# Optimization experiments

Hardware: AMD Instinct MI355X
Metric: run time of the kernel (lower is better)

Reference implementation:

```python
import jax, jax.numpy as jnp
import numpy as np

H = 1152      # embed_dim
NH = 16       # num heads
HD = H // NH  # head_dim = 72
SCALE = HD ** -0.5
B, S = 16, 729


def fake_quant(x, bits):
    """Symmetric per-tensor fake quantize-dequantize with straight-through estimator."""
    qmax = 2.0 ** (bits - 1) - 1.0
    scale = jnp.maximum(jnp.max(jnp.abs(x)), 1e-8) / qmax
    q = jnp.clip(jnp.round(x / scale), -qmax - 1.0, qmax) * scale
    return x + jax.lax.stop_gradient(q - x)  # STE


def fq_linear(x, W, b):
    # FakeQuantLinear: 8-bit fake-quant on activations and weights, fp accumulate
    return fake_quant(x, 8) @ fake_quant(W, 8).T + b


def setup_inputs() -> dict:
    key = jax.random.key(0)
    ks = jax.random.split(key, 9)
    std = H ** -0.5
    return {
        "hidden_states": jax.random.normal(ks[0], (B, S, H), jnp.float32),
        "Wq": jax.random.normal(ks[1], (H, H), jnp.float32) * std,
        "bq": jax.random.normal(ks[2], (H,), jnp.float32) * 0.02,
        "Wk": jax.random.normal(ks[3], (H, H), jnp.float32) * std,
        "bk": jax.random.normal(ks[4], (H,), jnp.float32) * 0.02,
        "Wv": jax.random.normal(ks[5], (H, H), jnp.float32) * std,
        "bv": jax.random.normal(ks[6], (H,), jnp.float32) * 0.02,
        "Wo": jax.random.normal(ks[7], (H, H), jnp.float32) * std,
        "bo": jax.random.normal(ks[8], (H,), jnp.float32) * 0.02,
    }


def reference(hidden_states, Wq, bq, Wk, bk, Wv, bv, Wo, bo):
    b, s, _ = hidden_states.shape
    q = fq_linear(hidden_states, Wq, bq).reshape(b, s, NH, HD).transpose(0, 2, 1, 3)
    k = fq_linear(hidden_states, Wk, bk).reshape(b, s, NH, HD).transpose(0, 2, 1, 3)
    v = fq_linear(hidden_states, Wv, bv).reshape(b, s, NH, HD).transpose(0, 2, 1, 3)
    # FakeQuantMatmul(8, 16): 8-bit quant on both matmul inputs, 16-bit quant on output
    attn = fake_quant(
        jnp.einsum("bhqd,bhkd->bhqk", fake_quant(q, 8), fake_quant(k, 8)), 16
    ) * SCALE
    # FakeQuantSoftmax(quant_bits=16): softmax then 16-bit fake quant
    attn = fake_quant(jax.nn.softmax(attn, axis=-1), 16)
    # FakeQuantMatmul(None, 8): no input quant, 8-bit output quant
    out = fake_quant(jnp.einsum("bhqk,bhkd->bhqd", attn, v), 8)
    out = out.transpose(0, 2, 1, 3).reshape(b, s, H)
    return fq_linear(out, Wo, bo)
```

## Files before the change

kernel.cpp:

```cpp
#include <hip/hip_runtime.h>
#include <math.h>

#define Hdim 1152
#define NHd  16
#define HDd  72
#define Bd   16
#define Sd   729
#define Ntok (Bd*Sd)
#define BHd  (Bd*NHd)
#define SCALE_F 0.117851130197757934f
#define LOG2E 1.44269504088896340736f

#define KFTB 8192
#define VFT 10240

#define SL_X 0
#define SL_WQ 1
#define SL_WK 2
#define SL_WV 3
#define SL_WO 4
#define SL_Q 5
#define SL_K 6
#define SL_LOGIT 8
#define SL_LMIN 9
#define SL_O 10

typedef short short8 __attribute__((ext_vector_type(8)));
typedef short short4v __attribute__((ext_vector_type(4)));
typedef float f32x4 __attribute__((ext_vector_type(4)));
typedef int int4v __attribute__((ext_vector_type(4)));

static __device__ __forceinline__ unsigned short f2bf(float f) {
  unsigned b = __float_as_uint(f);
  return (unsigned short)((b + 0x7FFFu + ((b >> 16) & 1u)) >> 16);
}
static __device__ __forceinline__ float bf2f(unsigned short u) {
  return __uint_as_float(((unsigned)u) << 16);
}
static __device__ __forceinline__ void atomicMaxF(float* p, float v) {
  atomicMax((unsigned int*)p, __float_as_uint(v));
}
static __device__ __forceinline__ void atomicMinF(float* p, float v) {
  atomicMin((unsigned int*)p, __float_as_uint(v));
}
static __device__ __forceinline__ float qscale(float mx, float qmax) {
  return fmaxf(mx, 1e-8f) / qmax;
}
static __device__ __forceinline__ float fexp2(float x) {
  float r; asm("v_exp_f32 %0, %1" : "=v"(r) : "v"(x)); return r;
}
static __device__ __forceinline__ float flog2(float x) {
  float r; asm("v_log_f32 %0, %1" : "=v"(r) : "v"(x)); return r;
}
static __device__ __forceinline__ short4v pack4(unsigned a, unsigned b, unsigned c, unsigned d) {
  union { unsigned u[2]; short4v s; } t;
  t.u[0] = a | (b << 16);
  t.u[1] = c | (d << 16);
  return t.s;
}
static __device__ __forceinline__ int q8i(float v, float s) {
  return (int)fminf(fmaxf(rintf(v / s), -128.f), 127.f);
}

#if __has_builtin(__builtin_amdgcn_mfma_f32_16x16x16bf16_1k)
#define MFMA16(a, b, c) __builtin_amdgcn_mfma_f32_16x16x16bf16_1k(a, b, c, 0, 0, 0)
#else
static __device__ __forceinline__ f32x4 MFMA16(short4v a, short4v b, f32x4 c) {
  asm("v_mfma_f32_16x16x16_bf16 %0, %1, %2, %0" : "+v"(c) : "v"(a), "v"(b));
  return c;
}
#endif
#if __has_builtin(__builtin_amdgcn_mfma_i32_16x16x64_i8)
#define MFMAI8(a, b, c) __builtin_amdgcn_mfma_i32_16x16x64_i8(a, b, c, 0, 0, 0)
#else
static __device__ __forceinline__ int4v MFMAI8(int4v a, int4v b, int4v c) {
  asm("v_mfma_i32_16x16x64_i8 %0, %1, %2, %0" : "+v"(c) : "v"(a), "v"(b));
  return c;
}
#endif

static __device__ __forceinline__ void gll16(const void* g, void* l) {
  __builtin_amdgcn_global_load_lds((const __attribute__((address_space(1))) void*)g,
                                   (__attribute__((address_space(3))) void*)l, 16, 0, 0);
}

__global__ void k_init(float* slots) {
  int i = threadIdx.x;
  if (i < 32) slots[i] = (i == SL_LMIN) ? __builtin_inff() : 0.0f;
}

__launch_bounds__(256)
__global__ void k_absmax(const float* __restrict__ X, const float* __restrict__ W0,
                         const float* __restrict__ W1, const float* __restrict__ W2,
                         const float* __restrict__ W3, float* slots) {
  int seg = blockIdx.y;
  const float* p; long n; int slot;
  if (seg == 0) { p = X; n = (long)Ntok * Hdim; slot = SL_X; }
  else {
    const float* ws4[4] = {W0, W1, W2, W3};
    p = ws4[seg - 1]; n = (long)Hdim * Hdim; slot = SL_WQ + seg - 1;
  }
  long n4 = n >> 2;
  const float4* p4 = (const float4*)p;
  float m = 0.f;
  for (long i = (long)blockIdx.x * blockDim.x + threadIdx.x; i < n4;
       i += (long)gridDim.x * blockDim.x) {
    float4 v = p4[i];
    m = fmaxf(m, fmaxf(fmaxf(fabsf(v.x), fabsf(v.y)), fmaxf(fabsf(v.z), fabsf(v.w))));
  }
  for (int off = 32; off; off >>= 1) m = fmaxf(m, __shfl_xor(m, off, 64));
  __shared__ float red[4];
  if ((threadIdx.x & 63) == 0) red[threadIdx.x >> 6] = m;
  __syncthreads();
  if (threadIdx.x == 0)
    atomicMaxF(&slots[slot], fmaxf(fmaxf(red[0], red[1]), fmaxf(red[2], red[3])));
}

__launch_bounds__(256)
__global__ void k_quant8i(const float* __restrict__ in, unsigned int* __restrict__ out,
                          long n, const float* __restrict__ slots, int slot) {
  float s = qscale(slots[slot], 127.0f);
  long n4 = n >> 2;
  const float4* in4 = (const float4*)in;
  for (long i = (long)blockIdx.x * blockDim.x + threadIdx.x; i < n4;
       i += (long)gridDim.x * blockDim.x) {
    float4 v = in4[i];
    unsigned a = (unsigned)q8i(v.x, s) & 255u;
    unsigned b = (unsigned)q8i(v.y, s) & 255u;
    unsigned c = (unsigned)q8i(v.z, s) & 255u;
    unsigned d = (unsigned)q8i(v.w, s) & 255u;
    out[i] = a | (b << 8) | (c << 16) | (d << 24);
  }
}

__launch_bounds__(256)
__global__ void k_quant8wi(const float* __restrict__ W0, const float* __restrict__ W1,
                           const float* __restrict__ W2, const float* __restrict__ W3,
                           unsigned int* O0, unsigned int* O1,
                           unsigned int* O2, unsigned int* O3,
                           const float* __restrict__ slots) {
  int seg = blockIdx.y;
  const float* ws4[4] = {W0, W1, W2, W3};
  unsigned int* os4[4] = {O0, O1, O2, O3};
  const float* in = ws4[seg];
  unsigned int* out = os4[seg];
  float s = qscale(slots[SL_WQ + seg], 127.0f);
  long n4 = ((long)Hdim * Hdim) >> 2;
  const float4* in4 = (const float4*)in;
  for (long i = (long)blockIdx.x * blockDim.x + threadIdx.x; i < n4;
       i += (long)gridDim.x * blockDim.x) {
    float4 v = in4[i];
    unsigned a = (unsigned)q8i(v.x, s) & 255u;
    unsigned b = (unsigned)q8i(v.y, s) & 255u;
    unsigned c = (unsigned)q8i(v.z, s) & 255u;
    unsigned d = (unsigned)q8i(v.w, s) & 255u;
    out[i] = a | (b << 8) | (c << 16) | (d << 24);
  }
}

#define GBM 128
#define GBN 128
#define GBK 64
__launch_bounds__(256, 3)
__global__ void k_gemm(const char* __restrict__ A,
                       const char* __restrict__ Bm,
                       const float* __restrict__ bias,
                       float* __restrict__ C,
                       float* slots, int slotA, int slotB, int slotOut) {
  __shared__ char As[GBM][GBK];
  __shared__ char Bs[GBN][GBK];
  __shared__ float red[4];
  int tid = threadIdx.x, lane = tid & 63, wid = tid >> 6;
  int wm = wid >> 1, wn = wid & 1;
  int l15 = lane & 15, l4 = lane >> 4;
  int bM = blockIdx.x, bN = blockIdx.y;
  int4v acc[4][4];
  for (int rf = 0; rf < 4; ++rf)
    for (int cf = 0; cf < 4; ++cf) acc[rf][cf] = int4v{0, 0, 0, 0};

  int srow = lane >> 2, scol = (lane & 3) * 16;
  const char* pa = A + ((long)(bM * GBM + wid * 32) + srow) * Hdim + scol;
  const char* pb = Bm + ((long)(bN * GBN + wid * 32) + srow) * Hdim + scol;

  for (int kt = 0; kt < Hdim / GBK; ++kt) {
    int kb = kt * GBK;
    __syncthreads();
    gll16(pa + kb, &As[wid * 32][0]);
    gll16(pa + kb + 16 * Hdim, &As[wid * 32 + 16][0]);
    gll16(pb + kb, &Bs[wid * 32][0]);
    gll16(pb + kb + 16 * Hdim, &Bs[wid * 32 + 16][0]);
    __syncthreads();
    int4v af[4], bf4[4];
#pragma unroll
    for (int rf = 0; rf < 4; ++rf) af[rf] = *(const int4v*)&As[wm * 64 + rf * 16 + l15][l4 * 16];
#pragma unroll
    for (int cf = 0; cf < 4; ++cf) bf4[cf] = *(const int4v*)&Bs[wn * 64 + cf * 16 + l15][l4 * 16];
#pragma unroll
    for (int rf = 0; rf < 4; ++rf)
#pragma unroll
      for (int cf = 0; cf < 4; ++cf)
        acc[rf][cf] = MFMAI8(af[rf], bf4[cf], acc[rf][cf]);
  }
  float alpha = qscale(slots[slotA], 127.f) * qscale(slots[slotB], 127.f);
  float lmax = 0.f;
#pragma unroll
  for (int cf = 0; cf < 4; ++cf) {
    int col = bN * GBN + wn * 64 + cf * 16 + l15;
    float bv = bias[col];
#pragma unroll
    for (int rf = 0; rf < 4; ++rf)
#pragma unroll
      for (int j = 0; j < 4; ++j) {
        int row = bM * GBM + wm * 64 + rf * 16 + l4 * 4 + j;
        if (row < Ntok) {
          float v = (float)acc[rf][cf][j] * alpha + bv;
          C[(long)row * Hdim + col] = v;
          lmax = fmaxf(lmax, fabsf(v));
        }
      }
  }
  if (slotOut >= 0) {
    for (int off = 32; off; off >>= 1) lmax = fmaxf(lmax, __shfl_xor(lmax, off, 64));
    if ((tid & 63) == 0) red[wid] = lmax;
    __syncthreads();
    if (tid == 0)
      atomicMaxF(&slots[slotOut], fmaxf(fmaxf(red[0], red[1]), fmaxf(red[2], red[3])));
  }
}

__launch_bounds__(256, 3)
__global__ void k_gemm3(const char* __restrict__ A,
                        const char* __restrict__ W0,
                        const char* __restrict__ W1,
                        const char* __restrict__ W2,
                        const float* __restrict__ b0, const float* __restrict__ b1,
                        const float* __restrict__ b2,
                        float* __restrict__ C0, float* __restrict__ C1,
                        float* __restrict__ C2, float* slots) {
  __shared__ char As[GBM][GBK];
  __shared__ char Bs[GBN][GBK];
  __shared__ float red[4];
  int bNg = blockIdx.y;
  int mi = bNg / 9, bN = bNg - mi * 9;
  const char* Bm = mi == 0 ? W0 : (mi == 1 ? W1 : W2);
  const float* bias = mi == 0 ? b0 : (mi == 1 ? b1 : b2);
  float* C = mi == 0 ? C0 : (mi == 1 ? C1 : C2);
  int slotB = SL_WQ + mi;
  int slotOut = mi == 0 ? SL_Q : (mi == 1 ? SL_K : -1);

  int tid = threadIdx.x, lane = tid & 63, wid = tid >> 6;
  int wm = wid >> 1, wn = wid & 1;
  int l15 = lane & 15, l4 = lane >> 4;
  int bM = blockIdx.x;
  int4v acc[4][4];
  for (int rf = 0; rf < 4; ++rf)
    for (int cf = 0; cf < 4; ++cf) acc[rf][cf] = int4v{0, 0, 0, 0};

  int srow = lane >> 2, scol = (lane & 3) * 16;
  const char* pa = A + ((long)(bM * GBM + wid * 32) + srow) * Hdim + scol;
  const char* pb = Bm + ((long)(bN * GBN + wid * 32) + srow) * Hdim + scol;

  for (int kt = 0; kt < Hdim / GBK; ++kt) {
    int kb = kt * GBK;
    __syncthreads();
    gll16(pa + kb, &As[wid * 32][0]);
    gll16(pa + kb + 16 * Hdim, &As[wid * 32 + 16][0]);
    gll16(pb + kb, &Bs[wid * 32][0]);
    gll16(pb + kb + 16 * Hdim, &Bs[wid * 32 + 16][0]);
    __syncthreads();
    int4v af[4], bf4[4];
#pragma unroll
    for (int rf = 0; rf < 4; ++rf) af[rf] = *(const int4v*)&As[wm * 64 + rf * 16 + l15][l4 * 16];
#pragma unroll
    for (int cf = 0; cf < 4; ++cf) bf4[cf] = *(const int4v*)&Bs[wn * 64 + cf * 16 + l15][l4 * 16];
#pragma unroll
    for (int rf = 0; rf < 4; ++rf)
#pragma unroll
      for (int cf = 0; cf < 4; ++cf)
        acc[rf][cf] = MFMAI8(af[rf], bf4[cf], acc[rf][cf]);
  }
  float alpha = qscale(slots[SL_X], 127.f) * qscale(slots[slotB], 127.f);
  float lmax = 0.f;
#pragma unroll
  for (int cf = 0; cf < 4; ++cf) {
    int col = bN * GBN + wn * 64 + cf * 16 + l15;
    float bv = bias[col];
#pragma unroll
    for (int rf = 0; rf < 4; ++rf)
#pragma unroll
      for (int j = 0; j < 4; ++j) {
        int row = bM * GBM + wm * 64 + rf * 16 + l4 * 4 + j;
        if (row < Ntok) {
          float v = (float)acc[rf][cf][j] * alpha + bv;
          C[(long)row * Hdim + col] = v;
          lmax = fmaxf(lmax, fabsf(v));
        }
      }
  }
  if (slotOut >= 0) {
    for (int off = 32; off; off >>= 1) lmax = fmaxf(lmax, __shfl_xor(lmax, off, 64));
    if ((tid & 63) == 0) red[wid] = lmax;
    __syncthreads();
    if (tid == 0)
      atomicMaxF(&slots[slotOut], fmaxf(fmaxf(red[0], red[1]), fmaxf(red[2], red[3])));
  }
}

__launch_bounds__(256)
__global__ void k_kfrag(const float* __restrict__ Kf, char* __restrict__ KF,
                        const float* __restrict__ slots) {
  int kt = blockIdx.x, bh = blockIdx.y;
  int b = bh >> 4, h = bh & 15;
  float s = qscale(slots[SL_K], 127.0f);
  int tid = threadIdx.x, lane = tid & 63, w = tid >> 6;
  int l15 = lane & 15, l4 = lane >> 4;
  long obase = ((long)(bh * 12 + kt)) * KFTB;
#pragma unroll
  for (int i = 0; i < 2; ++i) {
    int p = w * 2 + i;
    int cf = p >> 1, c = p & 1;
    int token = kt * 64 + cf * 16 + l15;
    char ov[16];
#pragma unroll
    for (int j = 0; j < 16; ++j) ov[j] = 0;
    if (token < Sd) {
      const float* src = &Kf[((long)(b * Sd + token)) * Hdim + h * HDd];
      if (c == 0) {
#pragma unroll
        for (int j = 0; j < 16; ++j) ov[j] = (char)q8i(src[l4 * 16 + j], s);
      } else if (l4 == 0) {
#pragma unroll
        for (int j = 0; j < 8; ++j) ov[j] = (char)q8i(src[64 + j], s);
      }
    }
    *(int4v*)&KF[obase + p * 1024 + lane * 16] = *(int4v*)ov;
  }
}

__launch_bounds__(256)
__global__ void k_vsplit(const float* __restrict__ Vf, unsigned short* __restrict__ VF) {
  int kt = blockIdx.x, bh = blockIdx.y;
  int b = bh >> 4, h = bh & 15;
  int tid = threadIdx.x, lane = tid & 63, w = tid >> 6;
  int l15 = lane & 15, l4 = lane >> 4;
  long obase = ((long)(bh * 12 + kt)) * VFT;
#pragma unroll
  for (int i = 0; i < 5; ++i) {
    int p = w + 4 * i;
    int dt = p >> 2, cf = p & 3;
    int d = dt * 16 + l15;
    int tok0 = kt * 64 + cf * 16 + l4 * 4;
    unsigned short u[8];
#pragma unroll
    for (int j = 0; j < 4; ++j) {
      int tok = tok0 + j;
      float v = 0.f;
      if (tok < Sd && d < HDd)
        v = Vf[((long)(b * Sd + tok)) * Hdim + h * HDd + d];
      unsigned short hb = f2bf(v);
      u[j] = hb;
      u[4 + j] = f2bf(v - bf2f(hb));
    }
    *(short8*)&VF[obase + (long)p * 512 + lane * 8] = *(short8*)u;
  }
}

static __device__ __forceinline__ void loadQ8(const char* __restrict__ Qq,
                                              int b, int h, int qc, int l4,
                                              int4v& qa, int4v& qb) {
  const char* qp = &Qq[((long)(b * Sd + qc)) * Hdim + h * HDd];
  union { long l[2]; int4v v; } u0, u1;
  u0.l[0] = *(const long*)(qp + l4 * 16);
  u0.l[1] = *(const long*)(qp + l4 * 16 + 8);
  qa = u0.v;
  u1.l[0] = (l4 == 0) ? *(const long*)(qp + 64) : 0L;
  u1.l[1] = 0L;
  qb = u1.v;
}

__launch_bounds__(256, 4)
__global__ void k_attnA(const char* __restrict__ Qq,
                        const char* __restrict__ KF, float* slots) {
  __shared__ float red[4];
  int qh = blockIdx.x, bh = blockIdx.y;
  int b = bh >> 4, h = bh & 15;
  int tid = threadIdx.x, lane = tid & 63, w = tid >> 6;
  int l15 = lane & 15, l4 = lane >> 4;
  const char* kfb = KF + (long)bh * 12 * KFTB;
  int4v qa[3], qb[3];
#pragma unroll
  for (int qs = 0; qs < 3; ++qs) {
    int qrow = (qh * 3 + qs) * 64 + w * 16 + l15;
    int qc = qrow > Sd - 1 ? Sd - 1 : qrow;
    loadQ8(Qq, b, h, qc, l4, qa[qs], qb[qs]);
  }
  float mx = 0.f;
#pragma unroll 1
  for (int kt = 0; kt < 12; ++kt) {
    int4v kf[8];
#pragma unroll
    for (int p = 0; p < 8; ++p)
      kf[p] = *(const int4v*)&kfb[(long)kt * KFTB + p * 1024 + lane * 16];
#pragma unroll
    for (int qs = 0; qs < 3; ++qs) {
#pragma unroll
      for (int cf = 0; cf < 4; ++cf) {
        int4v a = int4v{0, 0, 0, 0};
        a = MFMAI8(kf[cf * 2 + 0], qa[qs], a);
        a = MFMAI8(kf[cf * 2 + 1], qb[qs], a);
#pragma unroll
        for (int j = 0; j < 4; ++j) mx = fmaxf(mx, fabsf((float)a[j]));
      }
    }
  }
  mx *= qscale(slots[SL_Q], 127.f) * qscale(slots[SL_K], 127.f);
  for (int off = 32; off; off >>= 1) mx = fmaxf(mx, __shfl_xor(mx, off, 64));
  if ((tid & 63) == 0) red[w] = mx;
  __syncthreads();
  if (tid == 0)
    atomicMaxF(&slots[SL_LOGIT], fmaxf(fmaxf(red[0], red[1]), fmaxf(red[2], red[3])));
}

__launch_bounds__(256, 4)
__global__ void k_attnB(const char* __restrict__ Qq,
                        const char* __restrict__ KF, float* slots,
                        float* __restrict__ m_arr, float* __restrict__ l_arr) {
  __shared__ float red[4];
  int qh = blockIdx.x, bh = blockIdx.y;
  int b = bh >> 4, h = bh & 15;
  int tid = threadIdx.x, lane = tid & 63, w = tid >> 6;
  int l15 = lane & 15, l4 = lane >> 4;
  const char* kfb = KF + (long)bh * 12 * KFTB;
  int4v qa[3], qb[3];
#pragma unroll
  for (int qs = 0; qs < 3; ++qs) {
    int qrow = (qh * 3 + qs) * 64 + w * 16 + l15;
    int qc = qrow > Sd - 1 ? Sd - 1 : qrow;
    loadQ8(Qq, b, h, qc, l4, qa[qs], qb[qs]);
  }
  float s16 = qscale(slots[SL_LOGIT], 32767.f);
  float sqk = qscale(slots[SL_Q], 127.f) * qscale(slots[SL_K], 127.f);
  float c0 = sqk / s16;
  float c1e = s16 * SCALE_F * LOG2E;
  float m_run[3] = {-3.0e38f, -3.0e38f, -3.0e38f};
  float l_run[3] = {0.f, 0.f, 0.f};
#pragma unroll 1
  for (int kt = 0; kt < 12; ++kt) {
    int4v kf[8];
#pragma unroll
    for (int p = 0; p < 8; ++p)
      kf[p] = *(const int4v*)&kfb[(long)kt * KFTB + p * 1024 + lane * 16];
#pragma unroll
    for (int qs = 0; qs < 3; ++qs) {
      float nv[16];
#pragma unroll
      for (int cf = 0; cf < 4; ++cf) {
        int4v a = int4v{0, 0, 0, 0};
        a = MFMAI8(kf[cf * 2 + 0], qa[qs], a);
        a = MFMAI8(kf[cf * 2 + 1], qb[qs], a);
#pragma unroll
        for (int j = 0; j < 4; ++j) nv[cf * 4 + j] = rintf((float)a[j] * c0);
      }
      if (kt == 11) {
#pragma unroll
        for (int cf = 0; cf < 4; ++cf)
#pragma unroll
          for (int j = 0; j < 4; ++j) {
            int kcol = 704 + cf * 16 + l4 * 4 + j;
            if (kcol > Sd - 1) nv[cf * 4 + j] = -3.0e30f;
          }
      }
      float mt = nv[0];
#pragma unroll
      for (int i = 1; i < 16; ++i) mt = fmaxf(mt, nv[i]);
      mt = fmaxf(mt, __shfl_xor(mt, 16, 64));
      mt = fmaxf(mt, __shfl_xor(mt, 32, 64));
      float mn = fmaxf(m_run[qs], mt);
      float f = fexp2((m_run[qs] - mn) * c1e);
      float se = 0.f;
#pragma unroll
      for (int i = 0; i < 16; ++i) se += fexp2((nv[i] - mn) * c1e);
      se += __shfl_xor(se, 16, 64);
      se += __shfl_xor(se, 32, 64);
      l_run[qs] = l_run[qs] * f + se;
      m_run[qs] = mn;
    }
  }
  float lmin = 3.0e38f;
#pragma unroll
  for (int qs = 0; qs < 3; ++qs) {
    int qrow = (qh * 3 + qs) * 64 + w * 16 + l15;
    if (qrow < Sd) {
      if (l4 == 0) {
        m_arr[bh * Sd + qrow] = m_run[qs];
        l_arr[bh * Sd + qrow] = l_run[qs];
      }
      lmin = fminf(lmin, l_run[qs]);
    }
  }
  for (int off = 32; off; off >>= 1) lmin = fminf(lmin, __shfl_xor(lmin, off, 64));
  if ((tid & 63) == 0) red[w] = lmin;
  __syncthreads();
  if (tid == 0)
    atomicMinF(&slots[SL_LMIN], fminf(fminf(red[0], red[1]), fminf(red[2], red[3])));
}

__launch_bounds__(256, 5)
__global__ void k_attnC(const char* __restrict__ Qq,
                        const char* __restrict__ KF,
                        const unsigned short* __restrict__ VF,
                        const float* __restrict__ m_arr, const float* __restrict__ l_arr,
                        float* slots, float* __restrict__ O) {
  __shared__ char Ks[KFTB];
  __shared__ unsigned short Vs[VFT];
  __shared__ float red[4];
  int qp, bh;
  {
    int id = blockIdx.y * 6 + blockIdx.x;
    int xcd = id & 7, sub = id >> 3;
    int bhl = sub / 6;
    qp = sub - bhl * 6;
    bh = xcd * 32 + bhl;
  }
  int b = bh >> 4, h = bh & 15;
  int tid = threadIdx.x, lane = tid & 63, w = tid >> 6;
  int l15 = lane & 15, l4 = lane >> 4;
  float s16 = qscale(slots[SL_LOGIT], 32767.f);
  float sqk = qscale(slots[SL_Q], 127.f) * qscale(slots[SL_K], 127.f);
  float c0 = sqk / s16;
  float c1e = s16 * SCALE_F * LOG2E;
  float pmaxv = 1.0f / slots[SL_LMIN];
  float sp = fmaxf(pmaxv, 1e-8f) / 32767.0f;
  float inv_sp = 1.0f / sp;
  int4v qa[2], qb[2];
  float dexp[2];
#pragma unroll
  for (int qs = 0; qs < 2; ++qs) {
    int qrow = (qp * 2 + qs) * 64 + w * 16 + l15;
    int qc = qrow > Sd - 1 ? Sd - 1 : qrow;
    loadQ8(Qq, b, h, qc, l4, qa[qs], qb[qs]);
    float mn = m_arr[bh * Sd + qc];
    float c2 = (1.0f / l_arr[bh * Sd + qc]) * inv_sp;
    dexp[qs] = flog2(c2) - mn * c1e;
  }
  const char* kfb = KF + (long)bh * 12 * KFTB;
  const unsigned short* vfb = VF + (long)bh * 12 * VFT;
  f32x4 acc[2][5];
#pragma unroll
  for (int qs = 0; qs < 2; ++qs)
#pragma unroll
    for (int i = 0; i < 5; ++i) acc[qs][i] = f32x4{0.f, 0.f, 0.f, 0.f};

#pragma unroll 1
  for (int kt = 0; kt < 12; ++kt) {
    __syncthreads();
    {
      const char* kg = kfb + (long)kt * KFTB;
#pragma unroll
      for (int i = 0; i < 2; ++i) {
        int c = w * 2 + i;
        gll16(kg + c * 1024 + lane * 16, &Ks[c * 1024]);
      }
      const unsigned short* vg = vfb + (long)kt * VFT;
#pragma unroll
      for (int i = 0; i < 5; ++i) {
        int c = w + 4 * i;
        gll16(vg + c * 512 + lane * 8, &Vs[c * 512]);
      }
    }
    __syncthreads();
#pragma unroll
    for (int cf = 0; cf < 4; ++cf) {
      int4v k0 = *(const int4v*)&Ks[(cf * 2 + 0) * 1024 + lane * 16];
      int4v k1 = *(const int4v*)&Ks[(cf * 2 + 1) * 1024 + lane * 16];
      short4v Pp[2], Pr[2];
#pragma unroll
      for (int qs = 0; qs < 2; ++qs) {
        int4v a = int4v{0, 0, 0, 0};
        a = MFMAI8(k0, qa[qs], a);
        a = MFMAI8(k1, qb[qs], a);
        unsigned phb[4], rsb[4];
#pragma unroll
        for (int j = 0; j < 4; ++j) {
          float n = rintf((float)a[j] * c0);
          float nn = rintf(fexp2(fmaf(n, c1e, dexp[qs])));
          unsigned ub = __float_as_uint(nn);
          unsigned ph = (ub + 0x7FFFu + ((ub >> 16) & 1u)) >> 16;
          float rsf = nn - __uint_as_float(ph << 16);
          phb[j] = ph;
          rsb[j] = __float_as_uint(rsf) >> 16;
        }
        Pp[qs] = pack4(phb[0], phb[1], phb[2], phb[3]);
        Pr[qs] = pack4(rsb[0], rsb[1], rsb[2], rsb[3]);
      }
#pragma unroll
      for (int dt = 0; dt < 5; ++dt) {
        short8 vv = *(const short8*)&Vs[(dt * 4 + cf) * 512 + lane * 8];
        short4v vh = __builtin_shufflevector(vv, vv, 0, 1, 2, 3);
        short4v vl = __builtin_shufflevector(vv, vv, 4, 5, 6, 7);
#pragma unroll
        for (int qs = 0; qs < 2; ++qs) {
          acc[qs][dt] = MFMA16(Pp[qs], vh, acc[qs][dt]);
          acc[qs][dt] = MFMA16(Pp[qs], vl, acc[qs][dt]);
          acc[qs][dt] = MFMA16(Pr[qs], vh, acc[qs][dt]);
        }
      }
    }
  }
  float lmax = 0.f;
#pragma unroll
  for (int qs = 0; qs < 2; ++qs)
#pragma unroll
    for (int dt = 0; dt < 5; ++dt) {
      int d = dt * 16 + l15;
#pragma unroll
      for (int j = 0; j < 4; ++j) {
        int qr = (qp * 2 + qs) * 64 + w * 16 + l4 * 4 + j;
        if (qr < Sd && d < HDd) {
          float v = sp * acc[qs][dt][j];
          O[((long)(b * Sd + qr)) * Hdim + h * HDd + d] = v;
          lmax = fmaxf(lmax, fabsf(v));
        }
      }
    }
  for (int off = 32; off; off >>= 1) lmax = fmaxf(lmax, __shfl_xor(lmax, off, 64));
  if ((tid & 63) == 0) red[w] = lmax;
  __syncthreads();
  if (tid == 0)
    atomicMaxF(&slots[SL_O], fmaxf(fmaxf(red[0], red[1]), fmaxf(red[2], red[3])));
}

extern "C" void kernel_launch(void* const* d_in, const int* in_sizes, int n_in,
                              void* d_out, int out_size, void* d_ws, size_t ws_size,
                              hipStream_t stream) {
  const float* Xin = (const float*)d_in[0];
  const float* Wq = (const float*)d_in[1];
  const float* bq = (const float*)d_in[2];
  const float* Wk = (const float*)d_in[3];
  const float* bk = (const float*)d_in[4];
  const float* Wv = (const float*)d_in[5];
  const float* bv = (const float*)d_in[6];
  const float* Wo = (const float*)d_in[7];
  const float* bo = (const float*)d_in[8];
  float* out = (float*)d_out;
  char* ws = (char*)d_ws;

  size_t off = 0;
  auto alloc = [&](size_t bytes) {
    void* p = ws + off;
    off = (off + bytes + 255) & ~(size_t)255;
    return p;
  };
  float* slots = (float*)alloc(256);
  char* Xq  = (char*)alloc((size_t)Ntok * Hdim);
  char* Wqq = (char*)alloc((size_t)Hdim * Hdim);
  char* Wkq = (char*)alloc((size_t)Hdim * Hdim);
  char* Wvq = (char*)alloc((size_t)Hdim * Hdim);
  char* Woq = (char*)alloc((size_t)Hdim * Hdim);
  float* Kf = (float*)alloc((size_t)Ntok * Hdim * 4);
  float* Vf = (float*)alloc((size_t)Ntok * Hdim * 4);
  char* Qq = (char*)alloc((size_t)Ntok * Hdim);
  char* KFr = (char*)alloc((size_t)BHd * 12 * KFTB);
  unsigned short* VFr = (unsigned short*)alloc((size_t)BHd * 12 * VFT * 2);
  float* m_arr = (float*)alloc((size_t)BHd * Sd * 4);
  float* l_arr = (float*)alloc((size_t)BHd * Sd * 4);
  char* Oq = (char*)Vf;
  float* Qf = out;
  float* Of = out;

  k_init<<<1, 64, 0, stream>>>(slots);
  k_absmax<<<dim3(256, 5), 256, 0, stream>>>(Xin, Wq, Wk, Wv, Wo, slots);
  k_quant8i<<<1024, 256, 0, stream>>>(Xin, (unsigned int*)Xq, (long)Ntok * Hdim, slots, SL_X);
  k_quant8wi<<<dim3(128, 4), 256, 0, stream>>>(Wq, Wk, Wv, Wo, (unsigned int*)Wqq,
                                               (unsigned int*)Wkq, (unsigned int*)Wvq,
                                               (unsigned int*)Woq, slots);

  k_gemm3<<<dim3(92, 27), 256, 0, stream>>>(Xq, Wqq, Wkq, Wvq, bq, bk, bv,
                                            Qf, Kf, Vf, slots);

  k_quant8i<<<1024, 256, 0, stream>>>(Qf, (unsigned int*)Qq, (long)Ntok * Hdim, slots, SL_Q);
  k_kfrag<<<dim3(12, 256), 256, 0, stream>>>(Kf, KFr, slots);
  k_vsplit<<<dim3(12, 256), 256, 0, stream>>>(Vf, VFr);

  k_attnA<<<dim3(4, 256), 256, 0, stream>>>(Qq, KFr, slots);
  k_attnB<<<dim3(4, 256), 256, 0, stream>>>(Qq, KFr, slots, m_arr, l_arr);
  k_attnC<<<dim3(6, 256), 256, 0, stream>>>(Qq, KFr, VFr, m_arr, l_arr, slots, Of);

  k_quant8i<<<1024, 256, 0, stream>>>(Of, (unsigned int*)Oq, (long)Ntok * Hdim, slots, SL_O);
  k_gemm<<<dim3(92, 9), 256, 0, stream>>>(Oq, Woq, bo, out, slots, SL_O, SL_WO, -1);
}
```

Before: 491.0 us.

## Deepen int8 GEMM K-tile, enlarge attention query tiles, truncate bf16 split

The int8 GEMM core is factored into a shared helper. It now loads 128-wide K slices into a k-chunked LDS layout, which halves the number of barrier pairs and should make fragment reads conflict-free. The three attention kernels each process four 64-row query sub-tiles per block instead of two or three, so K/V fragment loads are reused across more queries and fewer blocks are launched. The hi/lo bf16 split of P now truncates instead of rounding, saving a few integer ops. The larger tiles raise register pressure and lower occupancy (attnC launch bounds drop from 5 to 3), and the tail blocks do more wasted work.

```diff
diff --git a/kernel.cpp b/kernel.cpp
--- a/kernel.cpp
+++ b/kernel.cpp
@@ -160,15 +160,55 @@
 
 #define GBM 128
 #define GBN 128
-#define GBK 64
+static __device__ __forceinline__ void gemm_core(const char* __restrict__ A,
+                                                 const char* __restrict__ Bm,
+                                                 int bM, int bN, int tid,
+                                                 char (*As)[4][GBM][16],
+                                                 char (*Bs)[4][GBN][16],
+                                                 int4v acc[4][4]) {
+  int lane = tid & 63, wid = tid >> 6;
+  int wm = wid >> 1, wn = wid & 1;
+  int l15 = lane & 15, l4 = lane >> 4;
+  const char* pa = A + ((long)(bM * GBM + lane)) * Hdim;
+  const char* pb = Bm + ((long)(bN * GBN + lane)) * Hdim;
+  for (int kt = 0; kt < 9; ++kt) {
+    int kb = kt * 128;
+    __syncthreads();
+#pragma unroll
+    for (int i = 0; i < 4; ++i) {
+      int c2 = wid * 4 + i;
+      int rg = c2 & 1, ks = (c2 >> 1) & 3, kc = c2 >> 3;
+      long go = (long)rg * 64 * Hdim + kb + kc * 64 + ks * 16;
+      gll16(pa + go, &As[kc][ks][rg * 64][0]);
+      gll16(pb + go, &Bs[kc][ks][rg * 64][0]);
+    }
+    __syncthreads();
+#pragma unroll
+    for (int kc = 0; kc < 2; ++kc) {
+      int4v af[4], bf4[4];
+#pragma unroll
+      for (int rf = 0; rf < 4; ++rf)
+        af[rf] = *(const int4v*)&As[kc][l4][wm * 64 + rf * 16 + l15][0];
+#pragma unroll
+      for (int cf = 0; cf < 4; ++cf)
+        bf4[cf] = *(const int4v*)&Bs[kc][l4][wn * 64 + cf * 16 + l15][0];
+#pragma unroll
+      for (int rf = 0; rf < 4; ++rf)
+#pragma unroll
+        for (int cf = 0; cf < 4; ++cf)
+          acc[rf][cf] = MFMAI8(af[rf], bf4[cf], acc[rf][cf]);
+    }
+  }
+}
+
 __launch_bounds__(256, 3)
 __global__ void k_gemm(const char* __restrict__ A,
                        const char* __restrict__ Bm,
                        const float* __restrict__ bias,
                        float* __restrict__ C,
                        float* slots, int slotA, int slotB, int slotOut) {
-  __shared__ char As[GBM][GBK];
-  __shared__ char Bs[GBN][GBK];
+  __shared__ char As[2][4][GBM][16];
+  __shared__ char Bs[2][4][GBN][16];
   __shared__ float red[4];
   int tid = threadIdx.x, lane = tid & 63, wid = tid >> 6;
   int wm = wid >> 1, wn = wid & 1;
@@ -177,30 +217,7 @@
   int4v acc[4][4];
   for (int rf = 0; rf < 4; ++rf)
     for (int cf = 0; cf < 4; ++cf) acc[rf][cf] = int4v{0, 0, 0, 0};
-
-  int srow = lane >> 2, scol = (lane & 3) * 16;
-  const char* pa = A + ((long)(bM * GBM + wid * 32) + srow) * Hdim + scol;
-  const char* pb = Bm + ((long)(bN * GBN + wid * 32) + srow) * Hdim + scol;
-
-  for (int kt = 0; kt < Hdim / GBK; ++kt) {
-    int kb = kt * GBK;
-    __syncthreads();
-    gll16(pa + kb, &As[wid * 32][0]);
-    gll16(pa + kb + 16 * Hdim, &As[wid * 32 + 16][0]);
-    gll16(pb + kb, &Bs[wid * 32][0]);
-    gll16(pb + kb + 16 * Hdim, &Bs[wid * 32 + 16][0]);
-    __syncthreads();
-    int4v af[4], bf4[4];
-#pragma unroll
-    for (int rf = 0; rf < 4; ++rf) af[rf] = *(const int4v*)&As[wm * 64 + rf * 16 + l15][l4 * 16];
-#pragma unroll
-    for (int cf = 0; cf < 4; ++cf) bf4[cf] = *(const int4v*)&Bs[wn * 64 + cf * 16 + l15][l4 * 16];
-#pragma unroll
-    for (int rf = 0; rf < 4; ++rf)
-#pragma unroll
-      for (int cf = 0; cf < 4; ++cf)
-        acc[rf][cf] = MFMAI8(af[rf], bf4[cf], acc[rf][cf]);
-  }
+  gemm_core(A, Bm, bM, bN, tid, As, Bs, acc);
   float alpha = qscale(slots[slotA], 127.f) * qscale(slots[slotB], 127.f);
   float lmax = 0.f;
 #pragma unroll
@@ -237,8 +254,8 @@
                         const float* __restrict__ b2,
                         float* __restrict__ C0, float* __restrict__ C1,
                         float* __restrict__ C2, float* slots) {
-  __shared__ char As[GBM][GBK];
-  __shared__ char Bs[GBN][GBK];
+  __shared__ char As[2][4][GBM][16];
+  __shared__ char Bs[2][4][GBN][16];
   __shared__ float red[4];
   int bNg = blockIdx.y;
   int mi = bNg / 9, bN = bNg - mi * 9;
@@ -255,30 +272,7 @@
   int4v acc[4][4];
   for (int rf = 0; rf < 4; ++rf)
     for (int cf = 0; cf < 4; ++cf) acc[rf][cf] = int4v{0, 0, 0, 0};
-
-  int srow = lane >> 2, scol = (lane & 3) * 16;
-  const char* pa = A + ((long)(bM * GBM + wid * 32) + srow) * Hdim + scol;
-  const char* pb = Bm + ((long)(bN * GBN + wid * 32) + srow) * Hdim + scol;
-
-  for (int kt = 0; kt < Hdim / GBK; ++kt) {
-    int kb = kt * GBK;
-    __syncthreads();
-    gll16(pa + kb, &As[wid * 32][0]);
-    gll16(pa + kb + 16 * Hdim, &As[wid * 32 + 16][0]);
-    gll16(pb + kb, &Bs[wid * 32][0]);
-    gll16(pb + kb + 16 * Hdim, &Bs[wid * 32 + 16][0]);
-    __syncthreads();
-    int4v af[4], bf4[4];
-#pragma unroll
-    for (int rf = 0; rf < 4; ++rf) af[rf] = *(const int4v*)&As[wm * 64 + rf * 16 + l15][l4 * 16];
-#pragma unroll
-    for (int cf = 0; cf < 4; ++cf) bf4[cf] = *(const int4v*)&Bs[wn * 64 + cf * 16 + l15][l4 * 16];
-#pragma unroll
-    for (int rf = 0; rf < 4; ++rf)
-#pragma unroll
-      for (int cf = 0; cf < 4; ++cf)
-        acc[rf][cf] = MFMAI8(af[rf], bf4[cf], acc[rf][cf]);
-  }
+  gemm_core(A, Bm, bM, bN, tid, As, Bs, acc);
   float alpha = qscale(slots[SL_X], 127.f) * qscale(slots[slotB], 127.f);
   float lmax = 0.f;
 #pragma unroll
@@ -387,10 +381,10 @@
   int tid = threadIdx.x, lane = tid & 63, w = tid >> 6;
   int l15 = lane & 15, l4 = lane >> 4;
   const char* kfb = KF + (long)bh * 12 * KFTB;
-  int4v qa[3], qb[3];
-#pragma unroll
-  for (int qs = 0; qs < 3; ++qs) {
-    int qrow = (qh * 3 + qs) * 64 + w * 16 + l15;
+  int4v qa[4], qb[4];
+#pragma unroll
+  for (int qs = 0; qs < 4; ++qs) {
+    int qrow = (qh * 4 + qs) * 64 + w * 16 + l15;
     int qc = qrow > Sd - 1 ? Sd - 1 : qrow;
     loadQ8(Qq, b, h, qc, l4, qa[qs], qb[qs]);
   }
@@ -402,7 +396,7 @@
     for (int p = 0; p < 8; ++p)
       kf[p] = *(const int4v*)&kfb[(long)kt * KFTB + p * 1024 + lane * 16];
 #pragma unroll
-    for (int qs = 0; qs < 3; ++qs) {
+    for (int qs = 0; qs < 4; ++qs) {
 #pragma unroll
       for (int cf = 0; cf < 4; ++cf) {
         int4v a = int4v{0, 0, 0, 0};
@@ -431,10 +425,10 @@
   int tid = threadIdx.x, lane = tid & 63, w = tid >> 6;
   int l15 = lane & 15, l4 = lane >> 4;
   const char* kfb = KF + (long)bh * 12 * KFTB;
-  int4v qa[3], qb[3];
-#pragma unroll
-  for (int qs = 0; qs < 3; ++qs) {
-    int qrow = (qh * 3 + qs) * 64 + w * 16 + l15;
+  int4v qa[4], qb[4];
+#pragma unroll
+  for (int qs = 0; qs < 4; ++qs) {
+    int qrow = (qh * 4 + qs) * 64 + w * 16 + l15;
     int qc = qrow > Sd - 1 ? Sd - 1 : qrow;
     loadQ8(Qq, b, h, qc, l4, qa[qs], qb[qs]);
   }
@@ -442,8 +436,8 @@
   float sqk = qscale(slots[SL_Q], 127.f) * qscale(slots[SL_K], 127.f);
   float c0 = sqk / s16;
   float c1e = s16 * SCALE_F * LOG2E;
-  float m_run[3] = {-3.0e38f, -3.0e38f, -3.0e38f};
-  float l_run[3] = {0.f, 0.f, 0.f};
+  float m_run[4] = {-3.0e38f, -3.0e38f, -3.0e38f, -3.0e38f};
+  float l_run[4] = {0.f, 0.f, 0.f, 0.f};
 #pragma unroll 1
   for (int kt = 0; kt < 12; ++kt) {
     int4v kf[8];
@@ -451,7 +445,7 @@
     for (int p = 0; p < 8; ++p)
       kf[p] = *(const int4v*)&kfb[(long)kt * KFTB + p * 1024 + lane * 16];
 #pragma unroll
-    for (int qs = 0; qs < 3; ++qs) {
+    for (int qs = 0; qs < 4; ++qs) {
       float nv[16];
 #pragma unroll
       for (int cf = 0; cf < 4; ++cf) {
@@ -488,8 +482,8 @@
   }
   float lmin = 3.0e38f;
 #pragma unroll
-  for (int qs = 0; qs < 3; ++qs) {
-    int qrow = (qh * 3 + qs) * 64 + w * 16 + l15;
+  for (int qs = 0; qs < 4; ++qs) {
+    int qrow = (qh * 4 + qs) * 64 + w * 16 + l15;
     if (qrow < Sd) {
       if (l4 == 0) {
         m_arr[bh * Sd + qrow] = m_run[qs];
@@ -505,7 +499,7 @@
     atomicMinF(&slots[SL_LMIN], fminf(fminf(red[0], red[1]), fminf(red[2], red[3])));
 }
 
-__launch_bounds__(256, 5)
+__launch_bounds__(256, 3)
 __global__ void k_attnC(const char* __restrict__ Qq,
                         const char* __restrict__ KF,
                         const unsigned short* __restrict__ VF,
@@ -516,10 +510,10 @@
   __shared__ float red[4];
   int qp, bh;
   {
-    int id = blockIdx.y * 6 + blockIdx.x;
+    int id = blockIdx.y * 3 + blockIdx.x;
     int xcd = id & 7, sub = id >> 3;
-    int bhl = sub / 6;
-    qp = sub - bhl * 6;
+    int bhl = sub / 3;
+    qp = sub - bhl * 3;
     bh = xcd * 32 + bhl;
   }
   int b = bh >> 4, h = bh & 15;
@@ -532,11 +526,11 @@
   float pmaxv = 1.0f / slots[SL_LMIN];
   float sp = fmaxf(pmaxv, 1e-8f) / 32767.0f;
   float inv_sp = 1.0f / sp;
-  int4v qa[2], qb[2];
-  float dexp[2];
-#pragma unroll
-  for (int qs = 0; qs < 2; ++qs) {
-    int qrow = (qp * 2 + qs) * 64 + w * 16 + l15;
+  int4v qa[4], qb[4];
+  float dexp[4];
+#pragma unroll
+  for (int qs = 0; qs < 4; ++qs) {
+    int qrow = (qp * 4 + qs) * 64 + w * 16 + l15;
     int qc = qrow > Sd - 1 ? Sd - 1 : qrow;
     loadQ8(Qq, b, h, qc, l4, qa[qs], qb[qs]);
     float mn = m_arr[bh * Sd + qc];
@@ -545,9 +539,9 @@
   }
   const char* kfb = KF + (long)bh * 12 * KFTB;
   const unsigned short* vfb = VF + (long)bh * 12 * VFT;
-  f32x4 acc[2][5];
-#pragma unroll
-  for (int qs = 0; qs < 2; ++qs)
+  f32x4 acc[4][5];
+#pragma unroll
+  for (int qs = 0; qs < 4; ++qs)
 #pragma unroll
     for (int i = 0; i < 5; ++i) acc[qs][i] = f32x4{0.f, 0.f, 0.f, 0.f};
 
@@ -573,9 +567,9 @@
     for (int cf = 0; cf < 4; ++cf) {
       int4v k0 = *(const int4v*)&Ks[(cf * 2 + 0) * 1024 + lane * 16];
       int4v k1 = *(const int4v*)&Ks[(cf * 2 + 1) * 1024 + lane * 16];
-      short4v Pp[2], Pr[2];
-#pragma unroll
-      for (int qs = 0; qs < 2; ++qs) {
+      short4v Pp[4], Pr[4];
+#pragma unroll
+      for (int qs = 0; qs < 4; ++qs) {
         int4v a = int4v{0, 0, 0, 0};
         a = MFMAI8(k0, qa[qs], a);
         a = MFMAI8(k1, qb[qs], a);
@@ -585,9 +579,9 @@
           float n = rintf((float)a[j] * c0);
           float nn = rintf(fexp2(fmaf(n, c1e, dexp[qs])));
           unsigned ub = __float_as_uint(nn);
-          unsigned ph = (ub + 0x7FFFu + ((ub >> 16) & 1u)) >> 16;
-          float rsf = nn - __uint_as_float(ph << 16);
-          phb[j] = ph;
+          unsigned hb = ub & 0xFFFF0000u;
+          float rsf = nn - __uint_as_float(hb);
+          phb[j] = hb >> 16;
           rsb[j] = __float_as_uint(rsf) >> 16;
         }
         Pp[qs] = pack4(phb[0], phb[1], phb[2], phb[3]);
@@ -599,7 +593,7 @@
         short4v vh = __builtin_shufflevector(vv, vv, 0, 1, 2, 3);
         short4v vl = __builtin_shufflevector(vv, vv, 4, 5, 6, 7);
 #pragma unroll
-        for (int qs = 0; qs < 2; ++qs) {
+        for (int qs = 0; qs < 4; ++qs) {
           acc[qs][dt] = MFMA16(Pp[qs], vh, acc[qs][dt]);
           acc[qs][dt] = MFMA16(Pp[qs], vl, acc[qs][dt]);
           acc[qs][dt] = MFMA16(Pr[qs], vh, acc[qs][dt]);
@@ -609,13 +603,13 @@
   }
   float lmax = 0.f;
 #pragma unroll
-  for (int qs = 0; qs < 2; ++qs)
+  for (int qs = 0; qs < 4; ++qs)
 #pragma unroll
     for (int dt = 0; dt < 5; ++dt) {
       int d = dt * 16 + l15;
 #pragma unroll
       for (int j = 0; j < 4; ++j) {
-        int qr = (qp * 2 + qs) * 64 + w * 16 + l4 * 4 + j;
+        int qr = (qp * 4 + qs) * 64 + w * 16 + l4 * 4 + j;
         if (qr < Sd && d < HDd) {
           float v = sp * acc[qs][dt][j];
           O[((long)(b * Sd + qr)) * Hdim + h * HDd + d] = v;
@@ -682,9 +676,9 @@
   k_kfrag<<<dim3(12, 256), 256, 0, stream>>>(Kf, KFr, slots);
   k_vsplit<<<dim3(12, 256), 256, 0, stream>>>(Vf, VFr);
 
-  k_attnA<<<dim3(4, 256), 256, 0, stream>>>(Qq, KFr, slots);
-  k_attnB<<<dim3(4, 256), 256, 0, stream>>>(Qq, KFr, slots, m_arr, l_arr);
-  k_attnC<<<dim3(6, 256), 256, 0, stream>>>(Qq, KFr, VFr, m_arr, l_arr, slots, Of);
+  k_attnA<<<dim3(3, 256), 256, 0, stream>>>(Qq, KFr, slots);
+  k_attnB<<<dim3(3, 256), 256, 0, stream>>>(Qq, KFr, slots, m_arr, l_arr);
+  k_attnC<<<dim3(3, 256), 256, 0, stream>>>(Qq, KFr, VFr, m_arr, l_arr, slots, Of);
 
   k_quant8i<<<1024, 256, 0, stream>>>(Of, (unsigned int*)Oq, (long)Ntok * Hdim, slots, SL_O);
   k_gemm<<<dim3(92, 9), 256, 0, stream>>>(Oq, Woq, bo, out, slots, SL_O, SL_WO, -1);
```

Measured after the change: 567.7 us. 15.6% more time.
